# Kernel optimization log

Hardware: AMD Instinct MI355X
Metric: run time of the kernel (lower is better)

The kernel has to match this reference:

```python
import math
import jax, jax.numpy as jnp
import numpy as np

N = 4096        # num nodes
IN_DIM = 512
H0 = 64         # hidden_dim[0]
H1 = 64         # hidden_dim[-1]
HEADS = 4
N_CLASSES = 10


def setup_inputs() -> dict:
    key = jax.random.key(0)
    ks = jax.random.split(key, 10)
    feats = jax.random.normal(ks[0], (N, IN_DIM), dtype=jnp.float32)
    counting_attn = jax.random.uniform(ks[1], (N, N), dtype=jnp.float32)
    s1 = 1.0 / math.sqrt(IN_DIM)
    s2 = 1.0 / math.sqrt(H0 * HEADS)
    # layer-1 heads, stacked: [H, out, in] (torch Linear weight layout)
    Wq1 = jax.random.normal(ks[2], (HEADS, H0, IN_DIM), dtype=jnp.float32) * s1
    Wk1 = jax.random.normal(ks[3], (HEADS, H0, IN_DIM), dtype=jnp.float32) * s1
    Wv1 = jax.random.normal(ks[4], (HEADS, H0, IN_DIM), dtype=jnp.float32) * s1
    # layer-2 single head: [out, in]
    Wq2 = jax.random.normal(ks[5], (H1, H0 * HEADS), dtype=jnp.float32) * s2
    Wk2 = jax.random.normal(ks[6], (H1, H0 * HEADS), dtype=jnp.float32) * s2
    Wv2 = jax.random.normal(ks[7], (H1, H0 * HEADS), dtype=jnp.float32) * s2
    Wc = jax.random.normal(ks[8], (N_CLASSES, H1), dtype=jnp.float32) * (1.0 / math.sqrt(H1))
    bc = jax.random.normal(ks[9], (N_CLASSES,), dtype=jnp.float32) * 0.01
    return {"feats": feats, "counting_attn": counting_attn,
            "Wq1": Wq1, "Wk1": Wk1, "Wv1": Wv1,
            "Wq2": Wq2, "Wk2": Wk2, "Wv2": Wv2,
            "Wc": Wc, "bc": bc}


def _gkat_heads(feat, Wq, Wk, Wv, counting):
    # feat: [N, in], Wq/Wk/Wv: [H, d, in], counting: [N, N] -> [N, H*d]
    Q = jnp.einsum('ni,hdi->hnd', feat, Wq)
    K = jnp.einsum('ni,hdi->hnd', feat, Wk)
    V = jnp.einsum('ni,hdi->hnd', feat, Wv)
    d = Q.shape[-1]
    logits = jnp.einsum('hnd,hmd->hnm', Q, K) / jnp.sqrt(jnp.asarray(d, Q.dtype))
    e = jnp.exp(logits - jnp.max(logits, axis=-1, keepdims=True))
    a = jnp.einsum('hnm,mk->hnk', e, counting)          # exp(logits) @ counting_attn
    a = a / (jnp.sum(a, axis=-1, keepdims=True) + 1e-9)  # row-normalize
    ret = jnp.einsum('hnm,hmd->hnd', a, V)
    ret = jax.nn.elu(ret)
    H, n, dd = ret.shape
    return jnp.transpose(ret, (1, 0, 2)).reshape(n, H * dd)  # concat heads along dim=1


def reference(feats, counting_attn, Wq1, Wk1, Wv1, Wq2, Wk2, Wv2, Wc, bc):
    # normalize over feature dim (torch.std is unbiased -> ddof=1)
    mean_ = jnp.mean(feats, axis=1, keepdims=True)
    std_ = jnp.std(feats, axis=1, keepdims=True, ddof=1)
    h = (feats - mean_) / (std_ + 1e-9)
    h = _gkat_heads(h, Wq1, Wk1, Wv1, counting_attn)                 # [N, H*H0]
    h = _gkat_heads(h, Wq2[None], Wk2[None], Wv2[None], counting_attn)  # [N, H1]
    return h @ Wc.T + bc
```

## Files before the change

kernel.cpp:

```cpp
#include <hip/hip_runtime.h>
#include <hip/hip_bf16.h>
#include <math.h>

#define NN4   4096
#define QSCALE 0.180336880111120420f

typedef __attribute__((ext_vector_type(8))) short short8;
typedef __attribute__((ext_vector_type(8))) unsigned short ushort8;
typedef __attribute__((ext_vector_type(4))) unsigned short ushort4v;
typedef __attribute__((ext_vector_type(4))) float f32x4;

__device__ __forceinline__ unsigned short f2b(float f) {
  union { __hip_bfloat16 h; unsigned short u; } v;
  v.h = __float2bfloat16(f);
  return v.u;
}
__device__ __forceinline__ float b2f(unsigned short s) {
  return __uint_as_float(((unsigned int)s) << 16);
}
__device__ __forceinline__ ushort8 cvt8(f32x4 a, f32x4 b) {
  return (ushort8){f2b(a[0]), f2b(a[1]), f2b(a[2]), f2b(a[3]),
                   f2b(b[0]), f2b(b[1]), f2b(b[2]), f2b(b[3])};
}

#define GLOAD16(gp, lp) __builtin_amdgcn_global_load_lds( \
    (const __attribute__((address_space(1))) void*)(gp),  \
    (__attribute__((address_space(3))) void*)(lp), 16, 0, 0)

__global__ __launch_bounds__(256) void k_norm(const float* __restrict__ x,
                                              unsigned short* __restrict__ y) {
  int row  = blockIdx.x * 4 + (threadIdx.x >> 6);
  int lane = threadIdx.x & 63;
  const float4* src = (const float4*)(x + (size_t)row * 512);
  float4 a = src[lane];
  float4 b = src[lane + 64];
  float s = a.x + a.y + a.z + a.w + b.x + b.y + b.z + b.w;
#pragma unroll
  for (int off = 32; off; off >>= 1) s += __shfl_xor(s, off);
  float mean = s * (1.0f / 512.0f);
  float ssq = 0.f, d;
  d = a.x - mean; ssq += d * d;  d = a.y - mean; ssq += d * d;
  d = a.z - mean; ssq += d * d;  d = a.w - mean; ssq += d * d;
  d = b.x - mean; ssq += d * d;  d = b.y - mean; ssq += d * d;
  d = b.z - mean; ssq += d * d;  d = b.w - mean; ssq += d * d;
#pragma unroll
  for (int off = 32; off; off >>= 1) ssq += __shfl_xor(ssq, off);
  float inv = 1.0f / (sqrtf(ssq * (1.0f / 511.0f)) + 1e-9f);
  unsigned short* dst = y + (size_t)row * 512;
  ushort4v va = (ushort4v){f2b((a.x - mean) * inv), f2b((a.y - mean) * inv),
                           f2b((a.z - mean) * inv), f2b((a.w - mean) * inv)};
  ushort4v vb = (ushort4v){f2b((b.x - mean) * inv), f2b((b.y - mean) * inv),
                           f2b((b.z - mean) * inv), f2b((b.w - mean) * inv)};
  *(ushort4v*)(dst + lane * 4)       = va;
  *(ushort4v*)(dst + 256 + lane * 4) = vb;
}

__global__ __launch_bounds__(256) void k_projqkv(
    const unsigned short* __restrict__ Ap, int K,
    const float* __restrict__ Wq, const float* __restrict__ Wk,
    const float* __restrict__ Wv, int N, int nT,
    unsigned short* __restrict__ Qo, unsigned short* __restrict__ Ko,
    unsigned short* __restrict__ VT, int padrows, float qscale) {
  __shared__ unsigned short As[128 * 40];
  __shared__ unsigned short Bs[128 * 40];
  const int tid = threadIdx.x;
  const int sel = blockIdx.y / nT;
  const int n0 = (blockIdx.y % nT) * 128;
  const int m0 = blockIdx.x * 128;
  const float* Bp = sel == 0 ? Wq : (sel == 1 ? Wk : Wv);
  const float bscale = sel == 0 ? qscale : 1.0f;
  const int lane = tid & 63, wid = tid >> 6;
  const int hi = lane >> 4, lo = lane & 15;
  const int wr = (wid >> 1) << 6, wc = (wid & 1) << 6;
  const int srow = tid >> 1, sk = (tid & 1) << 4;
  f32x4 acc[4][4];
#pragma unroll
  for (int i = 0; i < 4; ++i)
#pragma unroll
    for (int j = 0; j < 4; ++j) acc[i][j] = (f32x4){0.f, 0.f, 0.f, 0.f};

  for (int k0 = 0; k0 < K; k0 += 32) {
    ushort8 va0, va1, vb0, vb1;
    {
      const unsigned short* s = Ap + (size_t)(m0 + srow) * K + k0 + sk;
      va0 = *(const ushort8*)(s);
      va1 = *(const ushort8*)(s + 8);
    }
    {
      int gr = n0 + srow;
      if (gr < N) {
        const float* s = Bp + (size_t)gr * K + k0 + sk;
        f32x4 f0 = *(const f32x4*)(s) * bscale;
        f32x4 f1 = *(const f32x4*)(s + 4) * bscale;
        f32x4 f2 = *(const f32x4*)(s + 8) * bscale;
        f32x4 f3 = *(const f32x4*)(s + 12) * bscale;
        vb0 = cvt8(f0, f1); vb1 = cvt8(f2, f3);
      } else { vb0 = (ushort8)0; vb1 = (ushort8)0; }
    }
    __syncthreads();
    *(ushort8*)&As[srow * 40 + sk]     = va0;
    *(ushort8*)&As[srow * 40 + sk + 8] = va1;
    *(ushort8*)&Bs[srow * 40 + sk]     = vb0;
    *(ushort8*)&Bs[srow * 40 + sk + 8] = vb1;
    __syncthreads();
    short8 af[4], bf[4];
#pragma unroll
    for (int i = 0; i < 4; ++i)
      af[i] = *(const short8*)&As[(wr + (i << 4) + lo) * 40 + hi * 8];
#pragma unroll
    for (int j = 0; j < 4; ++j)
      bf[j] = *(const short8*)&Bs[(wc + (j << 4) + lo) * 40 + hi * 8];
#pragma unroll
    for (int i = 0; i < 4; ++i)
#pragma unroll
      for (int j = 0; j < 4; ++j)
        acc[i][j] = __builtin_amdgcn_mfma_f32_16x16x32_bf16(af[i], bf[j], acc[i][j], 0, 0, 0);
  }

  if (sel < 2) {
    unsigned short* Cp = sel == 0 ? Qo : Ko;
#pragma unroll
    for (int i = 0; i < 4; ++i)
#pragma unroll
      for (int j = 0; j < 4; ++j)
#pragma unroll
        for (int reg = 0; reg < 4; ++reg) {
          int r = m0 + wr + (i << 4) + (hi << 2) + reg;
          int c = n0 + wc + (j << 4) + lo;
          if (c < N) Cp[(size_t)r * N + c] = f2b(acc[i][j][reg]);
        }
  } else {
#pragma unroll
    for (int i = 0; i < 4; ++i)
#pragma unroll
      for (int j = 0; j < 4; ++j) {
        int c = n0 + wc + (j << 4) + lo;
        if (c < N) {
          int hh = c >> 6, dd = c & 63;
          int rb = m0 + wr + (i << 4) + (hi << 2);
          ushort4v pk = (ushort4v){f2b(acc[i][j][0]), f2b(acc[i][j][1]),
                                   f2b(acc[i][j][2]), f2b(acc[i][j][3])};
          *(ushort4v*)&VT[(size_t)(hh * 68 + dd) * NN4 + rb] = pk;
        }
      }
    int hstart = n0 >> 6;
    int hcnt = (N - n0) >> 6; if (hcnt > 2) hcnt = 2;
    int tot = hcnt * padrows * 128;
    for (int e = tid; e < tot; e += 256) {
      int hh = hstart + e / (padrows * 128);
      int rem = e % (padrows * 128);
      int j = rem >> 7, col = m0 + (rem & 127);
      VT[(size_t)(hh * 68 + 64 + j) * NN4 + col] = (j == 0) ? 0x3F80 : 0;
    }
  }
}

template<int NF>
__global__ __launch_bounds__(256, 2) void k_cvxg(
    const float* __restrict__ cnt,
    const unsigned short* __restrict__ Bt,
    unsigned short* __restrict__ Pb) {
  constexpr int LDB = NF * 16;
  __shared__ unsigned short As[2][128 * 40];
  __shared__ unsigned short Bs[2][LDB * 32];
  const int tid = threadIdx.x, lane = tid & 63, wid = tid >> 6;
  const int hi = lane >> 4, lo = lane & 15;
  const int m0 = blockIdx.x * 128;
  const int kbeg = blockIdx.y << 8, kend = kbeg + 256;
  const int arow = tid >> 1, ak = (tid & 1) << 4;
  const int boff = (lo * 64 + hi * 16) ^ (((lo >> 1) & 3) << 4);

  f32x4 acc[2][NF];
#pragma unroll
  for (int i = 0; i < 2; ++i)
#pragma unroll
    for (int j = 0; j < NF; ++j) acc[i][j] = (f32x4){0.f, 0.f, 0.f, 0.f};

  f32x4 ar0, ar1, ar2, ar3;
  {
    const float* s = cnt + (size_t)(m0 + arow) * 4096 + kbeg + ak;
    ar0 = *(const f32x4*)(s);     ar1 = *(const f32x4*)(s + 4);
    ar2 = *(const f32x4*)(s + 8); ar3 = *(const f32x4*)(s + 12);
  }
  for (int c = wid; c < NF; c += 4) {
    int P = c * 1024 + lane * 16;
    int L = P ^ ((P >> 3) & 0x30);
    GLOAD16(Bt + (size_t)(L >> 6) * 4096 + kbeg + ((L & 63) >> 1),
            (char*)&Bs[0][0] + c * 1024);
  }
  *(ushort8*)&As[0][arow * 40 + ak]     = cvt8(ar0, ar1);
  *(ushort8*)&As[0][arow * 40 + ak + 8] = cvt8(ar2, ar3);
  asm volatile("s_waitcnt vmcnt(0)" ::: "memory");
  __syncthreads();

  for (int k0 = kbeg; k0 < kend; k0 += 32) {
    const int cur = ((k0 - kbeg) >> 5) & 1, nxt = cur ^ 1;
    const bool more = (k0 + 32 < kend);
    if (more) {
      const float* s = cnt + (size_t)(m0 + arow) * 4096 + (k0 + 32) + ak;
      ar0 = *(const f32x4*)(s);     ar1 = *(const f32x4*)(s + 4);
      ar2 = *(const f32x4*)(s + 8); ar3 = *(const f32x4*)(s + 12);
      for (int c = wid; c < NF; c += 4) {
        int P = c * 1024 + lane * 16;
        int L = P ^ ((P >> 3) & 0x30);
        GLOAD16(Bt + (size_t)(L >> 6) * 4096 + (k0 + 32) + ((L & 63) >> 1),
                (char*)&Bs[nxt][0] + c * 1024);
      }
    }
    short8 af0 = *(const short8*)&As[cur][(32 * wid + lo) * 40 + hi * 8];
    short8 af1 = *(const short8*)&As[cur][(32 * wid + 16 + lo) * 40 + hi * 8];
    __builtin_amdgcn_s_setprio(1);
#pragma unroll
    for (int j = 0; j < NF; ++j) {
      short8 bf = *(const short8*)((const char*)&Bs[cur][0] + j * 1024 + boff);
      acc[0][j] = __builtin_amdgcn_mfma_f32_16x16x32_bf16(af0, bf, acc[0][j], 0, 0, 0);
      acc[1][j] = __builtin_amdgcn_mfma_f32_16x16x32_bf16(af1, bf, acc[1][j], 0, 0, 0);
    }
    __builtin_amdgcn_s_setprio(0);
    if (more) {
      *(ushort8*)&As[nxt][arow * 40 + ak]     = cvt8(ar0, ar1);
      *(ushort8*)&As[nxt][arow * 40 + ak + 8] = cvt8(ar2, ar3);
    }
    asm volatile("s_waitcnt vmcnt(0)" ::: "memory");
    __syncthreads();
  }
  unsigned short* P = Pb + (size_t)blockIdx.y * 4096 * LDB;
#pragma unroll
  for (int i = 0; i < 2; ++i)
#pragma unroll
    for (int j = 0; j < NF; ++j)
#pragma unroll
      for (int reg = 0; reg < 4; ++reg) {
        int r = m0 + 32 * wid + 16 * i + 4 * hi + reg;
        P[(size_t)r * LDB + 16 * j + lo] = f2b(acc[i][j][reg]);
      }
}

__global__ __launch_bounds__(256) void k_tredB(const unsigned short* __restrict__ in, int ld,
                                               int nsl, unsigned short* __restrict__ out,
                                               int orow) {
  __shared__ float t[64][65];
  const int n0 = blockIdx.x << 6, d0 = blockIdx.y << 6;
  const int o  = threadIdx.x & 7;
  const int rr = threadIdx.x >> 3;
  const size_t pstride = (size_t)4096 * ld;
  const bool valid = (o * 8) < (ld - d0);
#pragma unroll
  for (int pass = 0; pass < 2; ++pass) {
    const int r = rr + (pass << 5);
    float a[8] = {0.f, 0.f, 0.f, 0.f, 0.f, 0.f, 0.f, 0.f};
    if (valid) {
      const unsigned short* p = in + (size_t)(n0 + r) * ld + d0 + o * 8;
      for (int z = 0; z < nsl; ++z) {
        ushort8 v = *(const ushort8*)(p + (size_t)z * pstride);
#pragma unroll
        for (int k = 0; k < 8; ++k) a[k] += b2f(v[k]);
      }
    }
#pragma unroll
    for (int k = 0; k < 8; ++k) t[o * 8 + k][r] = a[k];
  }
  __syncthreads();
  const int c = threadIdx.x & 63, r4 = threadIdx.x >> 6;
#pragma unroll
  for (int i = 0; i < 16; ++i) {
    int dr = r4 + (i << 2);
    if (d0 + dr < orow)
      out[(size_t)(d0 + dr) * 4096 + n0 + c] = f2b(t[dr][c]);
  }
}

__global__ __launch_bounds__(256, 2) void k_attn(
    const unsigned short* __restrict__ Qg, const unsigned short* __restrict__ Kg,
    int ldqk, const unsigned short* __restrict__ CVg,
    unsigned short* __restrict__ Pb) {
  __shared__ unsigned short Ks[128 * 72];
  __shared__ unsigned short Cs[80 * 136];
  __shared__ unsigned short Es[128 * 136];
  const int tid = threadIdx.x, lane = tid & 63, wid = tid >> 6;
  const int hi = lane >> 4, lo = lane & 15;
  const int qb = blockIdx.x, h = blockIdx.y, sl = blockIdx.z;
  const int n0 = qb * 128;
  const int MS = 4096 / gridDim.z;
  const int m0beg = sl * MS;
  const int wr = (wid >> 1) << 6, wc = (wid & 1) << 6;

  short8 qf[4][2];
  const unsigned short* Qh = Qg + (size_t)h * 64;
#pragma unroll
  for (int j = 0; j < 4; ++j)
#pragma unroll
    for (int t = 0; t < 2; ++t)
      qf[j][t] = *(const short8*)(Qh + (size_t)(n0 + wc + 16 * j + lo) * ldqk + t * 32 + hi * 8);

  const unsigned short* CVh = CVg + (size_t)h * 68 * NN4;
  const unsigned short* Kh  = Kg + (size_t)h * 64;

  const int krow = tid >> 1, khalf = (tid & 1) << 5;
  int crdR[5], crdW[5], ccol[5];
#pragma unroll
  for (int k = 0; k < 5; ++k) {
    int c = tid + k * 256;
    int row = c >> 4;
    crdW[k] = row;
    crdR[k] = row < 68 ? row : 67;
    ccol[k] = (c & 15) << 3;
  }
  ushort8 krg[4], crg[5];

  auto LOADK = [&](int m0) {
    const unsigned short* src = Kh + (size_t)(m0 + krow) * ldqk + khalf;
    krg[0] = *(const ushort8*)(src);
    krg[1] = *(const ushort8*)(src + 8);
    krg[2] = *(const ushort8*)(src + 16);
    krg[3] = *(const ushort8*)(src + 24);
  };
  auto LOADC = [&](int m0) {
#pragma unroll
    for (int k = 0; k < 5; ++k)
      crg[k] = *(const ushort8*)(CVh + (size_t)crdR[k] * NN4 + m0 + ccol[k]);
  };
  auto WRITEK = [&]() {
    unsigned short* dp = &Ks[krow * 72 + khalf];
    *(ushort8*)(dp) = krg[0];      *(ushort8*)(dp + 8) = krg[1];
    *(ushort8*)(dp + 16) = krg[2]; *(ushort8*)(dp + 24) = krg[3];
  };
  auto WRITEC = [&]() {
#pragma unroll
    for (int k = 0; k < 5; ++k)
      *(ushort8*)&Cs[crdW[k] * 136 + ccol[k]] = crg[k];
  };

  f32x4 accn[2][5];
#pragma unroll
  for (int i = 0; i < 2; ++i)
#pragma unroll
    for (int j = 0; j < 5; ++j) accn[i][j] = (f32x4){0.f, 0.f, 0.f, 0.f};

  LOADK(m0beg); LOADC(m0beg);
  WRITEK(); WRITEC();
  __syncthreads();

  for (int mt = 0; mt < MS; mt += 128) {
    const int m0 = m0beg + mt;
    const bool more = (mt + 128) < MS;
    if (more) { LOADK(m0 + 128); LOADC(m0 + 128); }
    short8 kf[4][2];
#pragma unroll
    for (int i = 0; i < 4; ++i)
#pragma unroll
      for (int t = 0; t < 2; ++t)
        kf[i][t] = *(const short8*)&Ks[(wr + 16 * i + lo) * 72 + t * 32 + hi * 8];
    f32x4 s[4][4];
#pragma unroll
    for (int i = 0; i < 4; ++i)
#pragma unroll
      for (int j = 0; j < 4; ++j) s[i][j] = (f32x4){0.f, 0.f, 0.f, 0.f};
    __builtin_amdgcn_s_setprio(1);
#pragma unroll
    for (int t = 0; t < 2; ++t)
#pragma unroll
      for (int i = 0; i < 4; ++i)
#pragma unroll
        for (int j = 0; j < 4; ++j)
          s[i][j] = __builtin_amdgcn_mfma_f32_16x16x32_bf16(kf[i][t], qf[j][t], s[i][j], 0, 0, 0);
    __builtin_amdgcn_s_setprio(0);
#pragma unroll
    for (int i = 0; i < 4; ++i)
#pragma unroll
      for (int j = 0; j < 4; ++j) {
        unsigned int u0 = (unsigned int)f2b(__builtin_amdgcn_exp2f(s[i][j][0])) |
                          ((unsigned int)f2b(__builtin_amdgcn_exp2f(s[i][j][1])) << 16);
        unsigned int u1 = (unsigned int)f2b(__builtin_amdgcn_exp2f(s[i][j][2])) |
                          ((unsigned int)f2b(__builtin_amdgcn_exp2f(s[i][j][3])) << 16);
        unsigned long long pk = (unsigned long long)u0 | ((unsigned long long)u1 << 32);
        int row = wc + 16 * j + lo;
        int byte = row * 272 + (wr + 16 * i + 4 * hi) * 2;
        *(unsigned long long*)((char*)Es + (byte ^ ((row & 7) << 5))) = pk;
      }
    __syncthreads();
    if (more) WRITEK();
    __builtin_amdgcn_s_setprio(1);
#pragma unroll
    for (int t2 = 0; t2 < 4; ++t2) {
      int r0 = 32 * wid + lo, r1 = r0 + 16;
      int cb = (t2 * 32 + hi * 8) * 2;
      short8 ea0 = *(const short8*)((const char*)Es + ((r0 * 272 + cb) ^ ((r0 & 7) << 5)));
      short8 ea1 = *(const short8*)((const char*)Es + ((r1 * 272 + cb) ^ ((r1 & 7) << 5)));
      short8 cbv[5];
#pragma unroll
      for (int j2 = 0; j2 < 5; ++j2)
        cbv[j2] = *(const short8*)&Cs[(16 * j2 + lo) * 136 + t2 * 32 + hi * 8];
#pragma unroll
      for (int j2 = 0; j2 < 5; ++j2) {
        accn[0][j2] = __builtin_amdgcn_mfma_f32_16x16x32_bf16(ea0, cbv[j2], accn[0][j2], 0, 0, 0);
        accn[1][j2] = __builtin_amdgcn_mfma_f32_16x16x32_bf16(ea1, cbv[j2], accn[1][j2], 0, 0, 0);
      }
    }
    __builtin_amdgcn_s_setprio(0);
    __syncthreads();
    if (more) { WRITEC(); __syncthreads(); }
  }
  unsigned short* P = Pb + (((size_t)h * gridDim.x + qb) * gridDim.z + sl) * (128 * 80);
#pragma unroll
  for (int i2 = 0; i2 < 2; ++i2)
#pragma unroll
    for (int j2 = 0; j2 < 5; ++j2)
#pragma unroll
      for (int reg = 0; reg < 4; ++reg) {
        int r = 32 * wid + 16 * i2 + 4 * hi + reg;
        int c = 16 * j2 + lo;
        P[(size_t)r * 80 + c] = f2b(accn[i2][j2][reg]);
      }
}

__global__ void k_fin2(const unsigned short* __restrict__ parts, int nsl,
                       unsigned short* __restrict__ hb, int ldh) {
  int idx = blockIdx.x * 256 + threadIdx.x;
  int d = idx & 63, r = (idx >> 6) & 4095, h = idx >> 18;
  size_t b0 = ((size_t)(h * 32 + (r >> 7)) * nsl) * 10240 + (size_t)(r & 127) * 80;
  float nm = 0.f, dn = 0.f;
  for (int sl = 0; sl < nsl; ++sl) {
    const unsigned short* p = parts + b0 + (size_t)sl * 10240;
    nm += b2f(p[d]); dn += b2f(p[64]);
  }
  float x = nm / (dn + 1e-9f);
  x = x > 0.f ? x : expm1f(x);
  hb[(size_t)r * ldh + h * 64 + d] = f2b(x);
}

__global__ __launch_bounds__(256) void k_fincls(const unsigned short* __restrict__ parts,
                                                int nsl, const float* __restrict__ Wc,
                                                const float* __restrict__ bc,
                                                float* __restrict__ out) {
  int r = blockIdx.x * 4 + (threadIdx.x >> 6);
  int d = threadIdx.x & 63;
  size_t b0 = ((size_t)(r >> 7) * nsl) * 10240 + (size_t)(r & 127) * 80;
  float nm = 0.f, dn = 0.f;
  for (int sl = 0; sl < nsl; ++sl) {
    const unsigned short* p = parts + b0 + (size_t)sl * 10240;
    nm += b2f(p[d]); dn += b2f(p[64]);
  }
  float x = nm / (dn + 1e-9f);
  x = x > 0.f ? x : expm1f(x);
#pragma unroll
  for (int cl = 0; cl < 10; ++cl) {
    float v = x * Wc[cl * 64 + d];
#pragma unroll
    for (int off = 32; off; off >>= 1) v += __shfl_xor(v, off);
    if (d == 0) out[(size_t)r * 10 + cl] = v + bc[cl];
  }
}

extern "C" void kernel_launch(void* const* d_in, const int* in_sizes, int n_in,
                              void* d_out, int out_size, void* d_ws, size_t ws_size,
                              hipStream_t stream) {
  (void)in_sizes; (void)n_in; (void)out_size; (void)ws_size;
  const float* feats    = (const float*)d_in[0];
  const float* counting = (const float*)d_in[1];
  const float* Wq1 = (const float*)d_in[2];
  const float* Wk1 = (const float*)d_in[3];
  const float* Wv1 = (const float*)d_in[4];
  const float* Wq2 = (const float*)d_in[5];
  const float* Wk2 = (const float*)d_in[6];
  const float* Wv2 = (const float*)d_in[7];
  const float* Wc  = (const float*)d_in[8];
  const float* bc  = (const float*)d_in[9];
  float* out = (float*)d_out;

  char* w = (char*)d_ws;
  size_t off = 0;
  auto alloc = [&](size_t bytes) { void* p = w + off; off += (bytes + 255) & ~(size_t)255; return p; };
  unsigned short* hnb    = (unsigned short*)alloc((size_t)4096 * 512 * 2);
  unsigned short* Q1b    = (unsigned short*)alloc((size_t)4096 * 256 * 2);
  unsigned short* K1b    = (unsigned short*)alloc((size_t)4096 * 256 * 2);
  unsigned short* V1xT   = (unsigned short*)alloc((size_t)272 * 4096 * 2);
  unsigned short* CVX1Tb = (unsigned short*)alloc((size_t)272 * 4096 * 2);
  unsigned short* h1b    = (unsigned short*)alloc((size_t)4096 * 256 * 2);
  unsigned short* Q2b    = (unsigned short*)alloc((size_t)4096 * 64 * 2);
  unsigned short* K2b    = (unsigned short*)alloc((size_t)4096 * 64 * 2);
  unsigned short* V2xT   = (unsigned short*)alloc((size_t)80 * 4096 * 2);
  unsigned short* CVX2Tb = (unsigned short*)alloc((size_t)68 * 4096 * 2);
  unsigned short* big    = (unsigned short*)alloc((size_t)36 * 1024 * 1024);

  k_norm<<<1024, 256, 0, stream>>>(feats, hnb);

  k_projqkv<<<dim3(32, 6), 256, 0, stream>>>(hnb, 512, Wq1, Wk1, Wv1, 256, 2,
                                             Q1b, K1b, V1xT, 4, QSCALE);
  k_cvxg<17><<<dim3(32, 16), 256, 0, stream>>>(counting, V1xT, big);
  k_tredB<<<dim3(64, 5), 256, 0, stream>>>(big, 272, 16, CVX1Tb, 272);
  k_attn<<<dim3(32, 4, 4), 256, 0, stream>>>(Q1b, K1b, 256, CVX1Tb, big);
  k_fin2<<<4096, 256, 0, stream>>>(big, 4, h1b, 256);

  k_projqkv<<<dim3(32, 3), 256, 0, stream>>>(h1b, 256, Wq2, Wk2, Wv2, 64, 1,
                                             Q2b, K2b, V2xT, 16, QSCALE);
  k_cvxg<5><<<dim3(32, 16), 256, 0, stream>>>(counting, V2xT, big);
  k_tredB<<<dim3(64, 2), 256, 0, stream>>>(big, 80, 16, CVX2Tb, 68);
  k_attn<<<dim3(32, 1, 16), 256, 0, stream>>>(Q2b, K2b, 64, CVX2Tb, big);
  k_fincls<<<1024, 256, 0, stream>>>(big, 16, Wc, bc, out);
}
```

Before: 162.8 us.

## Read K and CV operands directly from global memory in attention kernel

```diff
diff --git a/kernel.cpp b/kernel.cpp
--- a/kernel.cpp
+++ b/kernel.cpp
@@ -270,12 +270,10 @@
   }
 }
 
-__global__ __launch_bounds__(256, 2) void k_attn(
+__global__ __launch_bounds__(256, 3) void k_attn(
     const unsigned short* __restrict__ Qg, const unsigned short* __restrict__ Kg,
     int ldqk, const unsigned short* __restrict__ CVg,
     unsigned short* __restrict__ Pb) {
-  __shared__ unsigned short Ks[128 * 72];
-  __shared__ unsigned short Cs[80 * 136];
   __shared__ unsigned short Es[128 * 136];
   const int tid = threadIdx.x, lane = tid & 63, wid = tid >> 6;
   const int hi = lane >> 4, lo = lane & 15;
@@ -296,61 +294,20 @@
   const unsigned short* CVh = CVg + (size_t)h * 68 * NN4;
   const unsigned short* Kh  = Kg + (size_t)h * 64;
 
-  const int krow = tid >> 1, khalf = (tid & 1) << 5;
-  int crdR[5], crdW[5], ccol[5];
-#pragma unroll
-  for (int k = 0; k < 5; ++k) {
-    int c = tid + k * 256;
-    int row = c >> 4;
-    crdW[k] = row;
-    crdR[k] = row < 68 ? row : 67;
-    ccol[k] = (c & 15) << 3;
-  }
-  ushort8 krg[4], crg[5];
-
-  auto LOADK = [&](int m0) {
-    const unsigned short* src = Kh + (size_t)(m0 + krow) * ldqk + khalf;
-    krg[0] = *(const ushort8*)(src);
-    krg[1] = *(const ushort8*)(src + 8);
-    krg[2] = *(const ushort8*)(src + 16);
-    krg[3] = *(const ushort8*)(src + 24);
-  };
-  auto LOADC = [&](int m0) {
-#pragma unroll
-    for (int k = 0; k < 5; ++k)
-      crg[k] = *(const ushort8*)(CVh + (size_t)crdR[k] * NN4 + m0 + ccol[k]);
-  };
-  auto WRITEK = [&]() {
-    unsigned short* dp = &Ks[krow * 72 + khalf];
-    *(ushort8*)(dp) = krg[0];      *(ushort8*)(dp + 8) = krg[1];
-    *(ushort8*)(dp + 16) = krg[2]; *(ushort8*)(dp + 24) = krg[3];
-  };
-  auto WRITEC = [&]() {
-#pragma unroll
-    for (int k = 0; k < 5; ++k)
-      *(ushort8*)&Cs[crdW[k] * 136 + ccol[k]] = crg[k];
-  };
-
   f32x4 accn[2][5];
 #pragma unroll
   for (int i = 0; i < 2; ++i)
 #pragma unroll
     for (int j = 0; j < 5; ++j) accn[i][j] = (f32x4){0.f, 0.f, 0.f, 0.f};
-
-  LOADK(m0beg); LOADC(m0beg);
-  WRITEK(); WRITEC();
-  __syncthreads();
 
   for (int mt = 0; mt < MS; mt += 128) {
     const int m0 = m0beg + mt;
-    const bool more = (mt + 128) < MS;
-    if (more) { LOADK(m0 + 128); LOADC(m0 + 128); }
     short8 kf[4][2];
 #pragma unroll
     for (int i = 0; i < 4; ++i)
 #pragma unroll
       for (int t = 0; t < 2; ++t)
-        kf[i][t] = *(const short8*)&Ks[(wr + 16 * i + lo) * 72 + t * 32 + hi * 8];
+        kf[i][t] = *(const short8*)(Kh + (size_t)(m0 + wr + 16 * i + lo) * ldqk + t * 32 + hi * 8);
     f32x4 s[4][4];
 #pragma unroll
     for (int i = 0; i < 4; ++i)
@@ -379,7 +336,6 @@
         *(unsigned long long*)((char*)Es + (byte ^ ((row & 7) << 5))) = pk;
       }
     __syncthreads();
-    if (more) WRITEK();
     __builtin_amdgcn_s_setprio(1);
 #pragma unroll
     for (int t2 = 0; t2 < 4; ++t2) {
@@ -390,7 +346,7 @@
       short8 cbv[5];
 #pragma unroll
       for (int j2 = 0; j2 < 5; ++j2)
-        cbv[j2] = *(const short8*)&Cs[(16 * j2 + lo) * 136 + t2 * 32 + hi * 8];
+        cbv[j2] = *(const short8*)(CVh + (size_t)(16 * j2 + lo) * NN4 + m0 + t2 * 32 + hi * 8);
 #pragma unroll
       for (int j2 = 0; j2 < 5; ++j2) {
         accn[0][j2] = __builtin_amdgcn_mfma_f32_16x16x32_bf16(ea0, cbv[j2], accn[0][j2], 0, 0, 0);
@@ -399,7 +355,6 @@
     }
     __builtin_amdgcn_s_setprio(0);
     __syncthreads();
-    if (more) { WRITEC(); __syncthreads(); }
   }
   unsigned short* P = Pb + (((size_t)h * gridDim.x + qb) * gridDim.z + sl) * (128 * 80);
 #pragma unroll
@@ -475,12 +430,12 @@
   unsigned short* Q1b    = (unsigned short*)alloc((size_t)4096 * 256 * 2);
   unsigned short* K1b    = (unsigned short*)alloc((size_t)4096 * 256 * 2);
   unsigned short* V1xT   = (unsigned short*)alloc((size_t)272 * 4096 * 2);
-  unsigned short* CVX1Tb = (unsigned short*)alloc((size_t)272 * 4096 * 2);
+  unsigned short* CVX1Tb = (unsigned short*)alloc((size_t)284 * 4096 * 2);
   unsigned short* h1b    = (unsigned short*)alloc((size_t)4096 * 256 * 2);
   unsigned short* Q2b    = (unsigned short*)alloc((size_t)4096 * 64 * 2);
   unsigned short* K2b    = (unsigned short*)alloc((size_t)4096 * 64 * 2);
   unsigned short* V2xT   = (unsigned short*)alloc((size_t)80 * 4096 * 2);
-  unsigned short* CVX2Tb = (unsigned short*)alloc((size_t)68 * 4096 * 2);
+  unsigned short* CVX2Tb = (unsigned short*)alloc((size_t)80 * 4096 * 2);
   unsigned short* big    = (unsigned short*)alloc((size_t)36 * 1024 * 1024);
 
   k_norm<<<1024, 256, 0, stream>>>(feats, hnb);
```

Measured after the change: 271.7 us. +66.9%, slower.

## Triple-buffer B tiles with partial vmcnt waits and trim a barrier

Applied to the files above, without the earlier changes.

```diff
diff --git a/kernel.cpp b/kernel.cpp
--- a/kernel.cpp
+++ b/kernel.cpp
@@ -162,11 +162,11 @@
     unsigned short* __restrict__ Pb) {
   constexpr int LDB = NF * 16;
   __shared__ unsigned short As[2][128 * 40];
-  __shared__ unsigned short Bs[2][LDB * 32];
+  __shared__ unsigned short Bs[3][NF * 512];
   const int tid = threadIdx.x, lane = tid & 63, wid = tid >> 6;
   const int hi = lane >> 4, lo = lane & 15;
   const int m0 = blockIdx.x * 128;
-  const int kbeg = blockIdx.y << 8, kend = kbeg + 256;
+  const int kbeg = blockIdx.y << 8;
   const int arow = tid >> 1, ak = (tid & 1) << 4;
   const int boff = (lo * 64 + hi * 16) ^ (((lo >> 1) & 3) << 4);
 
@@ -177,53 +177,60 @@
     for (int j = 0; j < NF; ++j) acc[i][j] = (f32x4){0.f, 0.f, 0.f, 0.f};
 
   f32x4 ar0, ar1, ar2, ar3;
-  {
-    const float* s = cnt + (size_t)(m0 + arow) * 4096 + kbeg + ak;
+  auto ALOAD = [&](int t) {
+    const float* s = cnt + (size_t)(m0 + arow) * 4096 + kbeg + t * 32 + ak;
     ar0 = *(const f32x4*)(s);     ar1 = *(const f32x4*)(s + 4);
     ar2 = *(const f32x4*)(s + 8); ar3 = *(const f32x4*)(s + 12);
-  }
-  for (int c = wid; c < NF; c += 4) {
-    int P = c * 1024 + lane * 16;
-    int L = P ^ ((P >> 3) & 0x30);
-    GLOAD16(Bt + (size_t)(L >> 6) * 4096 + kbeg + ((L & 63) >> 1),
-            (char*)&Bs[0][0] + c * 1024);
-  }
-  *(ushort8*)&As[0][arow * 40 + ak]     = cvt8(ar0, ar1);
-  *(ushort8*)&As[0][arow * 40 + ak + 8] = cvt8(ar2, ar3);
-  asm volatile("s_waitcnt vmcnt(0)" ::: "memory");
-  __syncthreads();
-
-  for (int k0 = kbeg; k0 < kend; k0 += 32) {
-    const int cur = ((k0 - kbeg) >> 5) & 1, nxt = cur ^ 1;
-    const bool more = (k0 + 32 < kend);
-    if (more) {
-      const float* s = cnt + (size_t)(m0 + arow) * 4096 + (k0 + 32) + ak;
-      ar0 = *(const f32x4*)(s);     ar1 = *(const f32x4*)(s + 4);
-      ar2 = *(const f32x4*)(s + 8); ar3 = *(const f32x4*)(s + 12);
-      for (int c = wid; c < NF; c += 4) {
-        int P = c * 1024 + lane * 16;
-        int L = P ^ ((P >> 3) & 0x30);
-        GLOAD16(Bt + (size_t)(L >> 6) * 4096 + (k0 + 32) + ((L & 63) >> 1),
-                (char*)&Bs[nxt][0] + c * 1024);
-      }
-    }
-    short8 af0 = *(const short8*)&As[cur][(32 * wid + lo) * 40 + hi * 8];
-    short8 af1 = *(const short8*)&As[cur][(32 * wid + 16 + lo) * 40 + hi * 8];
+  };
+  auto BSTAGE = [&](int t) {
+    for (int c = wid; c < NF; c += 4) {
+      int P = c * 1024 + lane * 16;
+      int L = P ^ ((P >> 3) & 0x30);
+      GLOAD16(Bt + (size_t)(L >> 6) * 4096 + kbeg + t * 32 + ((L & 63) >> 1),
+              (char*)&Bs[t % 3][0] + c * 1024);
+    }
+  };
+  auto AWRITE = [&](int t) {
+    *(ushort8*)&As[t & 1][arow * 40 + ak]     = cvt8(ar0, ar1);
+    *(ushort8*)&As[t & 1][arow * 40 + ak + 8] = cvt8(ar2, ar3);
+  };
+  auto WAITB = [&]() {
+    if constexpr (NF == 17) {
+      if (wid == 0) asm volatile("s_waitcnt vmcnt(5) lgkmcnt(0)" ::: "memory");
+      else          asm volatile("s_waitcnt vmcnt(4) lgkmcnt(0)" ::: "memory");
+    } else {
+      if (wid == 0) asm volatile("s_waitcnt vmcnt(2) lgkmcnt(0)" ::: "memory");
+      else          asm volatile("s_waitcnt vmcnt(1) lgkmcnt(0)" ::: "memory");
+    }
+  };
+
+  ALOAD(0);
+  BSTAGE(0);
+  BSTAGE(1);
+  AWRITE(0);
+  WAITB();
+  __builtin_amdgcn_s_barrier();
+  asm volatile("" ::: "memory");
+
+  for (int t = 0; t < 8; ++t) {
+    if (t + 1 < 8) ALOAD(t + 1);
+    if (t + 2 < 8) BSTAGE(t + 2);
+    short8 af0 = *(const short8*)&As[t & 1][(32 * wid + lo) * 40 + hi * 8];
+    short8 af1 = *(const short8*)&As[t & 1][(32 * wid + 16 + lo) * 40 + hi * 8];
     __builtin_amdgcn_s_setprio(1);
 #pragma unroll
     for (int j = 0; j < NF; ++j) {
-      short8 bf = *(const short8*)((const char*)&Bs[cur][0] + j * 1024 + boff);
+      short8 bf = *(const short8*)((const char*)&Bs[t % 3][0] + j * 1024 + boff);
       acc[0][j] = __builtin_amdgcn_mfma_f32_16x16x32_bf16(af0, bf, acc[0][j], 0, 0, 0);
       acc[1][j] = __builtin_amdgcn_mfma_f32_16x16x32_bf16(af1, bf, acc[1][j], 0, 0, 0);
     }
     __builtin_amdgcn_s_setprio(0);
-    if (more) {
-      *(ushort8*)&As[nxt][arow * 40 + ak]     = cvt8(ar0, ar1);
-      *(ushort8*)&As[nxt][arow * 40 + ak + 8] = cvt8(ar2, ar3);
-    }
-    asm volatile("s_waitcnt vmcnt(0)" ::: "memory");
-    __syncthreads();
-  }
+    if (t + 1 < 8) AWRITE(t + 1);
+    WAITB();
+    __builtin_amdgcn_s_barrier();
+    asm volatile("" ::: "memory");
+  }
+
   unsigned short* P = Pb + (size_t)blockIdx.y * 4096 * LDB;
 #pragma unroll
   for (int i = 0; i < 2; ++i)
@@ -399,7 +406,7 @@
     }
     __builtin_amdgcn_s_setprio(0);
     __syncthreads();
-    if (more) { WRITEC(); __syncthreads(); }
+    if (more) WRITEC();
   }
   unsigned short* P = Pb + (((size_t)h * gridDim.x + qb) * gridDim.z + sl) * (128 * 80);
 #pragma unroll
```

After: 163.5 us. No clear change (+0.4%).
